# Performance work log

Hardware: AMD Instinct MI355X
Metric: run time of the kernel (lower is better)

The kernel has to match this reference:

```python
import jax, jax.numpy as jnp
import numpy as np

N_HEADS = 16


def _apply_rope(x, cos, sin):
    # x: (B, T, H, hd); cos/sin: (max_len, hd//2)
    B, T, H, hd = x.shape
    c = cos[:T][None, :, None, :]  # (1, T, 1, hd//2)
    s = sin[:T][None, :, None, :]
    x1 = x[..., 0::2]
    x2 = x[..., 1::2]
    y1 = x1 * c - x2 * s
    y2 = x1 * s + x2 * c
    return jnp.stack((y1, y2), axis=-1).reshape(B, T, H, hd)


def _precompute_rope(head_dim, max_len):
    theta = 10000.0
    inv = 1.0 / theta ** (np.arange(0, head_dim, 2, dtype=np.float32) / head_dim)
    t = np.arange(max_len, dtype=np.float32)
    freqs = np.outer(t, inv)
    return jnp.asarray(np.cos(freqs)), jnp.asarray(np.sin(freqs))


def setup_inputs() -> dict:
    key = jax.random.key(0)
    k1, k2, k3 = jax.random.split(key, 3)
    B, T, C = 4, 2048, 2048
    hd = C // N_HEADS
    x = jax.random.normal(k1, (B, T, C), dtype=jnp.float32)
    w_attn = jax.random.normal(k2, (C, 3 * C), dtype=jnp.float32) * (C ** -0.5)
    w_proj = jax.random.normal(k3, (C, C), dtype=jnp.float32) * (C ** -0.5)
    rope_cos, rope_sin = _precompute_rope(hd, T)
    return {"x": x, "w_attn": w_attn, "w_proj": w_proj,
            "rope_cos": rope_cos, "rope_sin": rope_sin}


def reference(x, w_attn, w_proj, rope_cos, rope_sin):
    B, T, C = x.shape
    H = N_HEADS
    hd = C // H
    qkv = x @ w_attn  # (B, T, 3C)
    q, k, v = jnp.split(qkv, 3, axis=2)
    q = q.reshape(B, T, H, hd)
    k = k.reshape(B, T, H, hd)
    v = v.reshape(B, T, H, hd)
    q = _apply_rope(q, rope_cos, rope_sin)
    k = _apply_rope(k, rope_cos, rope_sin)
    scale = 1.0 / jnp.sqrt(jnp.asarray(hd, dtype=x.dtype))
    scores = jnp.einsum('bqhd,bkhd->bhqk', q, k) * scale  # (B, H, T, T)
    causal = jnp.tril(jnp.ones((T, T), dtype=bool))
    scores = jnp.where(causal[None, None], scores, jnp.finfo(scores.dtype).min)
    attn = jax.nn.softmax(scores, axis=-1)
    y = jnp.einsum('bhqk,bkhd->bqhd', attn, v).reshape(B, T, C)
    return y @ w_proj
```

## Files before the change

### kernel.cpp

```cpp
#include <hip/hip_runtime.h>
#include <cstdint>
#include <cstddef>

#define DEVI __device__ __forceinline__

typedef __attribute__((ext_vector_type(8))) short bf16x8;
typedef __attribute__((ext_vector_type(4))) float f32x4;

DEVI unsigned short f2bf(float f) {
  unsigned int u = __float_as_uint(f);
  u += 0x7fffu + ((u >> 16) & 1u);
  return (unsigned short)(u >> 16);
}
DEVI float bf2f(unsigned int us) { return __uint_as_float(us << 16); }

DEVI void gld_lds16(const void* g, void* l) {
  __builtin_amdgcn_global_load_lds(
      (const __attribute__((address_space(1))) void*)g,
      (__attribute__((address_space(3))) void*)l, 16, 0, 0);
}

__global__ __launch_bounds__(256) void k_conv(const float* __restrict__ in,
                                              short* __restrict__ out, int n4) {
  int i = blockIdx.x * 256 + threadIdx.x;
  if (i >= n4) return;
  float4 v = reinterpret_cast<const float4*>(in)[i];
  uint2 o;
  o.x = (unsigned)f2bf(v.x) | ((unsigned)f2bf(v.y) << 16);
  o.y = (unsigned)f2bf(v.z) | ((unsigned)f2bf(v.w) << 16);
  reinterpret_cast<uint2*>(out)[i] = o;
}

__global__ __launch_bounds__(256) void k_transpose(const float* __restrict__ in,
                                                   short* __restrict__ out,
                                                   int R, int Cc) {
  __shared__ short tile[64][66];
  int tcols = Cc >> 6;
  int tb = blockIdx.x % tcols;
  int rb = blockIdx.x / tcols;
  int tid = threadIdx.x;
#pragma unroll
  for (int rep = 0; rep < 16; ++rep) {
    int idx = rep * 256 + tid;
    int r = idx >> 6, c = idx & 63;
    tile[r][c] = (short)f2bf(in[(size_t)(rb * 64 + r) * Cc + tb * 64 + c]);
  }
  __syncthreads();
#pragma unroll
  for (int rep = 0; rep < 16; ++rep) {
    int idx = rep * 256 + tid;
    int r = idx >> 6, c = idx & 63;
    out[(size_t)(tb * 64 + r) * R + rb * 64 + c] = tile[c][r];
  }
}

template <typename OutT>
__global__ __launch_bounds__(512, 2) void k_gemm8(const short* __restrict__ A,
                                                  const short* __restrict__ BT,
                                                  OutT* __restrict__ C,
                                                  int M, int N, int K) {
  __shared__ short sA[4][8192];
  __shared__ short sB[4][8192];
  const int tid = threadIdx.x;
  const int wv = tid >> 6, lane = tid & 63;
  const int l16 = lane & 15, lhi = lane >> 4;
  const int wr = wv >> 2, wc = wv & 3;
  const int bm = blockIdx.x * 256, bn = blockIdx.y * 256;
  const int srow0 = wv * 16 + (lane >> 2);
  const int sgs = lane & 3;
  const int NT = K >> 5;

  auto stageA = [&](int kt, int b) {
#pragma unroll
    for (int j = 0; j < 2; ++j) {
      int row = j * 128 + srow0;
      int g = sgs ^ ((row >> 1) & 3);
      gld_lds16(A + (size_t)(bm + row) * K + kt + g * 8,
                &sA[b][j * 4096 + wv * 512]);
    }
  };
  auto stageB = [&](int kt, int b) {
#pragma unroll
    for (int j = 0; j < 2; ++j) {
      int row = j * 128 + srow0;
      int g = sgs ^ ((row >> 1) & 3);
      gld_lds16(BT + (size_t)(bn + row) * K + kt + g * 8,
                &sB[b][j * 4096 + wv * 512]);
    }
  };

  f32x4 acc[8][4] = {};
  bf16x8 aP[8], bP[4], aQ[8], bQ[4];

#define FRAG_READ(DA, DB, BUF)                                                 \
  {                                                                            \
    const short* bufA_ = sA[(BUF)];                                            \
    const short* bufB_ = sB[(BUF)];                                            \
    _Pragma("unroll") for (int n = 0; n < 4; ++n) {                            \
      int row = wc * 64 + n * 16 + l16;                                        \
      DB[n] = *(const bf16x8*)&bufB_[row * 32 + ((lhi ^ ((row >> 1) & 3)) << 3)]; \
    }                                                                          \
    _Pragma("unroll") for (int m = 0; m < 8; ++m) {                            \
      int row = wr * 128 + m * 16 + l16;                                       \
      DA[m] = *(const bf16x8*)&bufA_[row * 32 + ((lhi ^ ((row >> 1) & 3)) << 3)]; \
    }                                                                          \
  }

#define TILE_BODY(T, CA, CB, NA, NB)                                           \
  {                                                                            \
    const int t_ = (T);                                                        \
    if (t_ + 1 < NT) FRAG_READ(NA, NB, (t_ + 1) & 3);                          \
    if (t_ + 3 < NT) {                                                         \
      stageA((t_ + 3) * 32, (t_ + 3) & 3);                                     \
      stageB((t_ + 3) * 32, (t_ + 3) & 3);                                     \
    }                                                                          \
    __builtin_amdgcn_sched_barrier(0);                                         \
    if (t_ + 3 < NT) {                                                         \
      asm volatile("s_waitcnt vmcnt(4)" ::: "memory");                         \
    } else {                                                                   \
      asm volatile("s_waitcnt vmcnt(0)" ::: "memory");                         \
    }                                                                          \
    __builtin_amdgcn_sched_barrier(0);                                         \
    __builtin_amdgcn_s_setprio(1);                                             \
    _Pragma("unroll") for (int m = 0; m < 8; ++m)                              \
        _Pragma("unroll") for (int n = 0; n < 4; ++n)                          \
            acc[m][n] = __builtin_amdgcn_mfma_f32_16x16x32_bf16(               \
                CA[m], CB[n], acc[m][n], 0, 0, 0);                             \
    __builtin_amdgcn_s_setprio(0);                                             \
    __builtin_amdgcn_sched_barrier(0);                                         \
    __builtin_amdgcn_s_barrier();                                              \
    __builtin_amdgcn_sched_barrier(0);                                         \
  }

  stageA(0, 0); stageB(0, 0);
  stageA(32, 1); stageB(32, 1);
  stageA(64, 2); stageB(64, 2);
  asm volatile("s_waitcnt vmcnt(8)" ::: "memory");
  __builtin_amdgcn_s_barrier();
  FRAG_READ(aP, bP, 0);
  asm volatile("s_waitcnt vmcnt(4)" ::: "memory");
  __builtin_amdgcn_s_barrier();
  __builtin_amdgcn_sched_barrier(0);

  for (int t = 0; t < NT; t += 2) {
    TILE_BODY(t, aP, bP, aQ, bQ);
    TILE_BODY(t + 1, aQ, bQ, aP, bP);
  }
#undef FRAG_READ
#undef TILE_BODY

#pragma unroll
  for (int m = 0; m < 8; ++m) {
#pragma unroll
    for (int n = 0; n < 4; ++n) {
      int col = bn + wc * 64 + n * 16 + l16;
#pragma unroll
      for (int r = 0; r < 4; ++r) {
        int row = bm + wr * 128 + m * 16 + lhi * 4 + r;
        if constexpr (sizeof(OutT) == 2)
          C[(size_t)row * N + col] = (OutT)f2bf(acc[m][n][r]);
        else
          C[(size_t)row * N + col] = acc[m][n][r];
      }
    }
  }
}

__global__ __launch_bounds__(256) void k_rope(const short* __restrict__ qkv,
                                              const float* __restrict__ cosb,
                                              const float* __restrict__ sinb,
                                              short* __restrict__ Qr,
                                              short* __restrict__ Kr) {
  const float kC = 0.08838834764831845f * 1.44269504088896340f;
  int gid = blockIdx.x * 4 + (threadIdx.x >> 6);
  int lane = threadIdx.x & 63;
  int h = gid & 15;
  int bt = gid >> 4;
  int t = bt & 2047;
  int b = bt >> 11;
  float c = cosb[t * 64 + lane];
  float s = sinb[t * 64 + lane];
  size_t qidx = (size_t)bt * 6144 + h * 128 + 2 * lane;
  size_t oidx = ((size_t)(b * 16 + h) * 2048 + t) * 128 + 2 * lane;
  unsigned int qp = *reinterpret_cast<const unsigned int*>(qkv + qidx);
  {
    float x1 = bf2f(qp & 0xffffu), x2 = bf2f(qp >> 16);
    unsigned int o = (unsigned)f2bf((x1 * c - x2 * s) * kC) |
                     ((unsigned)f2bf((x1 * s + x2 * c) * kC) << 16);
    *reinterpret_cast<unsigned int*>(Qr + oidx) = o;
  }
  unsigned int kp = *reinterpret_cast<const unsigned int*>(qkv + qidx + 2048);
  {
    float x1 = bf2f(kp & 0xffffu), x2 = bf2f(kp >> 16);
    unsigned int o = (unsigned)f2bf(x1 * c - x2 * s) |
                     ((unsigned)f2bf(x1 * s + x2 * c) << 16);
    *reinterpret_cast<unsigned int*>(Kr + oidx) = o;
  }
}

__global__ __launch_bounds__(256) void k_vtrans(const short* __restrict__ qkv,
                                                short* __restrict__ VT) {
  __shared__ short tile[64][66];
  int bh = blockIdx.x;
  int t0 = blockIdx.y * 64;
  int d0 = blockIdx.z * 64;
  int b = bh >> 4, h = bh & 15;
  int tid = threadIdx.x;
#pragma unroll
  for (int rep = 0; rep < 16; ++rep) {
    int idx = rep * 256 + tid;
    int r = idx >> 6, c = idx & 63;
    tile[r][c] = qkv[(size_t)(b * 2048 + t0 + r) * 6144 + 4096 + h * 128 + d0 + c];
  }
  __syncthreads();
#pragma unroll
  for (int rep = 0; rep < 16; ++rep) {
    int idx = rep * 256 + tid;
    int r = idx >> 6, c = idx & 63;
    VT[(size_t)(bh * 128 + d0 + r) * 2048 + t0 + c] = tile[c][r];
  }
}

__global__ __launch_bounds__(256) void k_attn(const short* __restrict__ Qr,
                                              const short* __restrict__ Kr,
                                              const short* __restrict__ VT,
                                              short* __restrict__ Y) {
  __shared__ short sK[2][64 * 128];
  __shared__ short sVT[2][128 * 64];
  __shared__ short sP[4][16 * 64];
  const int tid = threadIdx.x, wv = tid >> 6, lane = tid & 63;
  const int l8r = lane >> 3, l8c = lane & 7, l16 = lane & 15, lhi = lane >> 4;
  const int bid = blockIdx.x;
  const int pair = bid & 15, bh = bid >> 4;
  const size_t base = (size_t)bh * 2048 * 128;
  const int b = bh >> 4, h = bh & 15;

  const short ob = (short)0x3F80;
  const bf16x8 ones = {ob, ob, ob, ob, ob, ob, ob, ob};

  auto stage = [&](int kv0, int buf) {
#pragma unroll
    for (int rr = 0; rr < 4; ++rr) {
      int ch = rr * 4 + wv;
      {
        int row = ch * 4 + lhi;
        int wch = l16 ^ (row & 7);
        gld_lds16(Kr + base + (size_t)(kv0 + row) * 128 + wch * 8,
                  &sK[buf][ch * 512]);
      }
      {
        int drow = ch * 8 + l8r;
        int wch = l8c ^ (drow & 7);
        gld_lds16(VT + base + (size_t)drow * 2048 + kv0 + wch * 8,
                  &sVT[buf][ch * 512]);
      }
    }
  };

  for (int half = 0; half < 2; ++half) {
    const int qt = half ? 31 - pair : pair;
    const int q0 = qt * 64;
    const int nt = qt + 1;

    bf16x8 qf[4];
    const int qrow = q0 + wv * 16 + l16;
#pragma unroll
    for (int ks = 0; ks < 4; ++ks)
      qf[ks] = *reinterpret_cast<const bf16x8*>(Qr + base + (size_t)qrow * 128 +
                                                ks * 32 + lhi * 8);

    f32x4 acc_o[8] = {};
    f32x4 acc_l = {};
    float m_run[4];
#pragma unroll
    for (int r = 0; r < 4; ++r) m_run[r] = -1e30f;

    stage(0, 0);
    __syncthreads();

    for (int it = 0; it < nt; ++it) {
      const int cur = it & 1;
      if (it + 1 < nt) stage((it + 1) * 64, cur ^ 1);

      f32x4 sacc[4] = {};
#pragma unroll
      for (int cf = 0; cf < 4; ++cf) {
        int krow = cf * 16 + l16;
#pragma unroll
        for (int ks = 0; ks < 4; ++ks) {
          int e = krow * 128 + ks * 32 + lhi * 8;
          bf16x8 kf = *reinterpret_cast<const bf16x8*>(
              &sK[cur][e ^ ((krow & 7) << 3)]);
          sacc[cf] = __builtin_amdgcn_mfma_f32_16x16x32_bf16(qf[ks], kf,
                                                             sacc[cf], 0, 0, 0);
        }
      }

      if (it == nt - 1) {
#pragma unroll
        for (int cf = 0; cf < 4; ++cf) {
          int col = cf * 16 + l16;
#pragma unroll
          for (int r = 0; r < 4; ++r)
            if (col > wv * 16 + lhi * 4 + r) sacc[cf][r] = -3e38f;
        }
      }

      bool exceed = false;
#pragma unroll
      for (int cf = 0; cf < 4; ++cf)
#pragma unroll
        for (int r = 0; r < 4; ++r)
          exceed |= (sacc[cf][r] > m_run[r] + 8.f);

      if (__any(exceed)) {
        float resc[4];
#pragma unroll
        for (int r = 0; r < 4; ++r) {
          float mx = fmaxf(fmaxf(sacc[0][r], sacc[1][r]),
                           fmaxf(sacc[2][r], sacc[3][r]));
          mx = fmaxf(mx, __shfl_xor(mx, 1));
          mx = fmaxf(mx, __shfl_xor(mx, 2));
          mx = fmaxf(mx, __shfl_xor(mx, 4));
          mx = fmaxf(mx, __shfl_xor(mx, 8));
          float mnew = fmaxf(m_run[r], mx);
          resc[r] = exp2f(m_run[r] - mnew);
          m_run[r] = mnew;
        }
#pragma unroll
        for (int df = 0; df < 8; ++df)
#pragma unroll
          for (int r = 0; r < 4; ++r) acc_o[df][r] *= resc[r];
#pragma unroll
        for (int r = 0; r < 4; ++r) acc_l[r] *= resc[r];
      }

#pragma unroll
      for (int cf = 0; cf < 4; ++cf)
#pragma unroll
        for (int r = 0; r < 4; ++r) {
          float p = exp2f(sacc[cf][r] - m_run[r]);
          int prow = lhi * 4 + r;
          int e = prow * 64 + cf * 16 + l16;
          sP[wv][e ^ ((prow & 7) << 3)] = (short)f2bf(p);
        }

#pragma unroll
      for (int kk = 0; kk < 2; ++kk) {
        int e = l16 * 64 + kk * 32 + lhi * 8;
        bf16x8 pa = *reinterpret_cast<const bf16x8*>(
            &sP[wv][e ^ ((l16 & 7) << 3)]);
        acc_l = __builtin_amdgcn_mfma_f32_16x16x32_bf16(pa, ones, acc_l, 0, 0, 0);
#pragma unroll
        for (int df = 0; df < 8; ++df) {
          int vrow = df * 16 + l16;
          int ev = vrow * 64 + kk * 32 + lhi * 8;
          bf16x8 vb = *reinterpret_cast<const bf16x8*>(
              &sVT[cur][ev ^ ((vrow & 7) << 3)]);
          acc_o[df] = __builtin_amdgcn_mfma_f32_16x16x32_bf16(pa, vb,
                                                              acc_o[df], 0, 0, 0);
        }
      }
      __syncthreads();
    }

    float inv[4];
#pragma unroll
    for (int r = 0; r < 4; ++r) inv[r] = 1.f / acc_l[r];
#pragma unroll
    for (int df = 0; df < 8; ++df) {
      int col = h * 128 + df * 16 + l16;
#pragma unroll
      for (int r = 0; r < 4; ++r) {
        int row = q0 + wv * 16 + lhi * 4 + r;
        Y[((size_t)b * 2048 + row) * 2048 + col] =
            (short)f2bf(acc_o[df][r] * inv[r]);
      }
    }
  }
}

extern "C" void kernel_launch(void* const* d_in, const int* in_sizes, int n_in,
                              void* d_out, int out_size, void* d_ws, size_t ws_size,
                              hipStream_t stream) {
  const float* x        = (const float*)d_in[0];
  const float* w_attn   = (const float*)d_in[1];
  const float* w_proj   = (const float*)d_in[2];
  const float* rope_cos = (const float*)d_in[3];
  const float* rope_sin = (const float*)d_in[4];

  char* ws = (char*)d_ws;
  short* xbf    = (short*)(ws);
  short* wattnT = (short*)(ws + 33554432ull);
  short* wprojT = (short*)(ws + 58720256ull);
  short* qkv    = (short*)(ws + 67108864ull);
  short* Y      = qkv;
  short* Qr     = (short*)(ws + 167772160ull);
  short* Kr     = (short*)(ws + 201326592ull);
  short* VT     = (short*)(ws + 234881024ull);

  k_conv<<<16384, 256, 0, stream>>>(x, xbf, 4194304);
  k_transpose<<<3072, 256, 0, stream>>>(w_attn, wattnT, 2048, 6144);
  k_transpose<<<1024, 256, 0, stream>>>(w_proj, wprojT, 2048, 2048);
  k_gemm8<short><<<dim3(32, 24), 512, 0, stream>>>(xbf, wattnT, qkv,
                                                   8192, 6144, 2048);
  k_rope<<<32768, 256, 0, stream>>>(qkv, rope_cos, rope_sin, Qr, Kr);
  k_vtrans<<<dim3(64, 32, 2), 256, 0, stream>>>(qkv, VT);
  k_attn<<<1024, 256, 0, stream>>>(Qr, Kr, VT, Y);
  k_gemm8<float><<<dim3(32, 8), 512, 0, stream>>>(Y, wprojT, (float*)d_out,
                                                  8192, 2048, 2048);
}
```

Measured before the change: 496.0 us.

## Double query tile per attention block so each wave handles 32 query rows

```diff
diff --git a/kernel.cpp b/kernel.cpp
--- a/kernel.cpp
+++ b/kernel.cpp
@@ -227,11 +227,11 @@
                                               short* __restrict__ Y) {
   __shared__ short sK[2][64 * 128];
   __shared__ short sVT[2][128 * 64];
-  __shared__ short sP[4][16 * 64];
+  __shared__ short sP[4][32 * 64];
   const int tid = threadIdx.x, wv = tid >> 6, lane = tid & 63;
   const int l8r = lane >> 3, l8c = lane & 7, l16 = lane & 15, lhi = lane >> 4;
   const int bid = blockIdx.x;
-  const int pair = bid & 15, bh = bid >> 4;
+  const int pair = bid & 7, bh = bid >> 3;
   const size_t base = (size_t)bh * 2048 * 128;
   const int b = bh >> 4, h = bh & 15;
 
@@ -258,22 +258,27 @@
   };
 
   for (int half = 0; half < 2; ++half) {
-    const int qt = half ? 31 - pair : pair;
-    const int q0 = qt * 64;
-    const int nt = qt + 1;
-
-    bf16x8 qf[4];
-    const int qrow = q0 + wv * 16 + l16;
-#pragma unroll
-    for (int ks = 0; ks < 4; ++ks)
-      qf[ks] = *reinterpret_cast<const bf16x8*>(Qr + base + (size_t)qrow * 128 +
-                                                ks * 32 + lhi * 8);
-
-    f32x4 acc_o[8] = {};
-    f32x4 acc_l = {};
-    float m_run[4];
-#pragma unroll
-    for (int r = 0; r < 4; ++r) m_run[r] = -1e30f;
+    const int qt = half ? 15 - pair : pair;
+    const int q0 = qt * 128;
+    const int nt = 2 * qt + 2;
+
+    bf16x8 qf[2][4];
+#pragma unroll
+    for (int v = 0; v < 2; ++v) {
+      const int qrow = q0 + wv * 32 + v * 16 + l16;
+#pragma unroll
+      for (int ks = 0; ks < 4; ++ks)
+        qf[v][ks] = *reinterpret_cast<const bf16x8*>(
+            Qr + base + (size_t)qrow * 128 + ks * 32 + lhi * 8);
+    }
+
+    f32x4 acc_o[2][8] = {};
+    f32x4 acc_l[2] = {};
+    float m_run[2][4];
+#pragma unroll
+    for (int v = 0; v < 2; ++v)
+#pragma unroll
+      for (int r = 0; r < 4; ++r) m_run[v][r] = -1e30f;
 
     stage(0, 0);
     __syncthreads();
@@ -282,7 +287,7 @@
       const int cur = it & 1;
       if (it + 1 < nt) stage((it + 1) * 64, cur ^ 1);
 
-      f32x4 sacc[4] = {};
+      f32x4 sacc[2][4] = {};
 #pragma unroll
       for (int cf = 0; cf < 4; ++cf) {
         int krow = cf * 16 + l16;
@@ -291,90 +296,113 @@
           int e = krow * 128 + ks * 32 + lhi * 8;
           bf16x8 kf = *reinterpret_cast<const bf16x8*>(
               &sK[cur][e ^ ((krow & 7) << 3)]);
-          sacc[cf] = __builtin_amdgcn_mfma_f32_16x16x32_bf16(qf[ks], kf,
-                                                             sacc[cf], 0, 0, 0);
+          sacc[0][cf] = __builtin_amdgcn_mfma_f32_16x16x32_bf16(qf[0][ks], kf,
+                                                                sacc[0][cf], 0, 0, 0);
+          sacc[1][cf] = __builtin_amdgcn_mfma_f32_16x16x32_bf16(qf[1][ks], kf,
+                                                                sacc[1][cf], 0, 0, 0);
         }
       }
 
-      if (it == nt - 1) {
-#pragma unroll
-        for (int cf = 0; cf < 4; ++cf) {
-          int col = cf * 16 + l16;
+      if (it >= nt - 2) {
+        const int rel = it * 64 - q0;
+#pragma unroll
+        for (int v = 0; v < 2; ++v)
+#pragma unroll
+          for (int cf = 0; cf < 4; ++cf) {
+            int col = rel + cf * 16 + l16;
+#pragma unroll
+            for (int r = 0; r < 4; ++r)
+              if (col > wv * 32 + v * 16 + lhi * 4 + r) sacc[v][cf][r] = -3e38f;
+          }
+      }
+
+      bool exceed = false;
+#pragma unroll
+      for (int v = 0; v < 2; ++v)
+#pragma unroll
+        for (int cf = 0; cf < 4; ++cf)
 #pragma unroll
           for (int r = 0; r < 4; ++r)
-            if (col > wv * 16 + lhi * 4 + r) sacc[cf][r] = -3e38f;
+            exceed |= (sacc[v][cf][r] > m_run[v][r] + 8.f);
+
+      if (__any(exceed)) {
+#pragma unroll
+        for (int v = 0; v < 2; ++v) {
+          float resc[4];
+#pragma unroll
+          for (int r = 0; r < 4; ++r) {
+            float mx = fmaxf(fmaxf(sacc[v][0][r], sacc[v][1][r]),
+                             fmaxf(sacc[v][2][r], sacc[v][3][r]));
+            mx = fmaxf(mx, __shfl_xor(mx, 1));
+            mx = fmaxf(mx, __shfl_xor(mx, 2));
+            mx = fmaxf(mx, __shfl_xor(mx, 4));
+            mx = fmaxf(mx, __shfl_xor(mx, 8));
+            float mnew = fmaxf(m_run[v][r], mx);
+            resc[r] = exp2f(m_run[v][r] - mnew);
+            m_run[v][r] = mnew;
+          }
+#pragma unroll
+          for (int df = 0; df < 8; ++df)
+#pragma unroll
+            for (int r = 0; r < 4; ++r) acc_o[v][df][r] *= resc[r];
+#pragma unroll
+          for (int r = 0; r < 4; ++r) acc_l[v][r] *= resc[r];
         }
       }
 
-      bool exceed = false;
-#pragma unroll
-      for (int cf = 0; cf < 4; ++cf)
-#pragma unroll
-        for (int r = 0; r < 4; ++r)
-          exceed |= (sacc[cf][r] > m_run[r] + 8.f);
-
-      if (__any(exceed)) {
-        float resc[4];
-#pragma unroll
-        for (int r = 0; r < 4; ++r) {
-          float mx = fmaxf(fmaxf(sacc[0][r], sacc[1][r]),
-                           fmaxf(sacc[2][r], sacc[3][r]));
-          mx = fmaxf(mx, __shfl_xor(mx, 1));
-          mx = fmaxf(mx, __shfl_xor(mx, 2));
-          mx = fmaxf(mx, __shfl_xor(mx, 4));
-          mx = fmaxf(mx, __shfl_xor(mx, 8));
-          float mnew = fmaxf(m_run[r], mx);
-          resc[r] = exp2f(m_run[r] - mnew);
-          m_run[r] = mnew;
+#pragma unroll
+      for (int v = 0; v < 2; ++v)
+#pragma unroll
+        for (int cf = 0; cf < 4; ++cf)
+#pragma unroll
+          for (int r = 0; r < 4; ++r) {
+            float p = exp2f(sacc[v][cf][r] - m_run[v][r]);
+            int prow = v * 16 + lhi * 4 + r;
+            int e = prow * 64 + cf * 16 + l16;
+            sP[wv][e ^ ((prow & 7) << 3)] = (short)f2bf(p);
+          }
+
+#pragma unroll
+      for (int kk = 0; kk < 2; ++kk) {
+        bf16x8 pa[2];
+#pragma unroll
+        for (int v = 0; v < 2; ++v) {
+          int prow = v * 16 + l16;
+          int e = prow * 64 + kk * 32 + lhi * 8;
+          pa[v] = *reinterpret_cast<const bf16x8*>(
+              &sP[wv][e ^ ((prow & 7) << 3)]);
+          acc_l[v] = __builtin_amdgcn_mfma_f32_16x16x32_bf16(pa[v], ones,
+                                                             acc_l[v], 0, 0, 0);
         }
-#pragma unroll
-        for (int df = 0; df < 8; ++df)
-#pragma unroll
-          for (int r = 0; r < 4; ++r) acc_o[df][r] *= resc[r];
-#pragma unroll
-        for (int r = 0; r < 4; ++r) acc_l[r] *= resc[r];
-      }
-
-#pragma unroll
-      for (int cf = 0; cf < 4; ++cf)
-#pragma unroll
-        for (int r = 0; r < 4; ++r) {
-          float p = exp2f(sacc[cf][r] - m_run[r]);
-          int prow = lhi * 4 + r;
-          int e = prow * 64 + cf * 16 + l16;
-          sP[wv][e ^ ((prow & 7) << 3)] = (short)f2bf(p);
-        }
-
-#pragma unroll
-      for (int kk = 0; kk < 2; ++kk) {
-        int e = l16 * 64 + kk * 32 + lhi * 8;
-        bf16x8 pa = *reinterpret_cast<const bf16x8*>(
-            &sP[wv][e ^ ((l16 & 7) << 3)]);
-        acc_l = __builtin_amdgcn_mfma_f32_16x16x32_bf16(pa, ones, acc_l, 0, 0, 0);
 #pragma unroll
         for (int df = 0; df < 8; ++df) {
           int vrow = df * 16 + l16;
           int ev = vrow * 64 + kk * 32 + lhi * 8;
           bf16x8 vb = *reinterpret_cast<const bf16x8*>(
               &sVT[cur][ev ^ ((vrow & 7) << 3)]);
-          acc_o[df] = __builtin_amdgcn_mfma_f32_16x16x32_bf16(pa, vb,
-                                                              acc_o[df], 0, 0, 0);
+          acc_o[0][df] = __builtin_amdgcn_mfma_f32_16x16x32_bf16(pa[0], vb,
+                                                                 acc_o[0][df], 0, 0, 0);
+          acc_o[1][df] = __builtin_amdgcn_mfma_f32_16x16x32_bf16(pa[1], vb,
+                                                                 acc_o[1][df], 0, 0, 0);
         }
       }
       __syncthreads();
     }
 
-    float inv[4];
-#pragma unroll
-    for (int r = 0; r < 4; ++r) inv[r] = 1.f / acc_l[r];
-#pragma unroll
-    for (int df = 0; df < 8; ++df) {
-      int col = h * 128 + df * 16 + l16;
-#pragma unroll
-      for (int r = 0; r < 4; ++r) {
-        int row = q0 + wv * 16 + lhi * 4 + r;
-        Y[((size_t)b * 2048 + row) * 2048 + col] =
-            (short)f2bf(acc_o[df][r] * inv[r]);
+#pragma unroll
+    for (int v = 0; v < 2; ++v) {
+      float inv[4];
+#pragma unroll
+      for (int r = 0; r < 4; ++r) inv[r] = 1.f / acc_l[v][r];
+#pragma unroll
+      for (int df = 0; df < 8; ++df) {
+        int col = h * 128 + df * 16 + l16;
+#pragma unroll
+        for (int r = 0; r < 4; ++r) {
+          int row = q0 + wv * 32 + v * 16 + lhi * 4 + r;
+          Y[((size_t)b * 2048 + row) * 2048 + col] =
+              (short)f2bf(acc_o[v][df][r] * inv[r]);
+        }
       }
     }
   }
@@ -406,7 +434,7 @@
                                                    8192, 6144, 2048);
   k_rope<<<32768, 256, 0, stream>>>(qkv, rope_cos, rope_sin, Qr, Kr);
   k_vtrans<<<dim3(64, 32, 2), 256, 0, stream>>>(qkv, VT);
-  k_attn<<<1024, 256, 0, stream>>>(Qr, Kr, VT, Y);
+  k_attn<<<512, 256, 0, stream>>>(Qr, Kr, VT, Y);
   k_gemm8<float><<<dim3(32, 8), 512, 0, stream>>>(Y, wprojT, (float*)d_out,
                                                   8192, 2048, 2048);
 }
```

After: 521.7 us. 5.2% more time.

## Fuse RoPE and V transpose into the QKV GEMM epilogue

Applied to the files above, without the earlier changes.

```diff
diff --git a/kernel.cpp b/kernel.cpp
--- a/kernel.cpp
+++ b/kernel.cpp
@@ -54,11 +54,16 @@
   }
 }
 
-template <typename OutT>
+template <int MODE, typename OutT>
 __global__ __launch_bounds__(512, 2) void k_gemm8(const short* __restrict__ A,
                                                   const short* __restrict__ BT,
                                                   OutT* __restrict__ C,
-                                                  int M, int N, int K) {
+                                                  int M, int N, int K,
+                                                  const float* __restrict__ cosb,
+                                                  const float* __restrict__ sinb,
+                                                  short* __restrict__ Qr,
+                                                  short* __restrict__ Kr,
+                                                  short* __restrict__ VT) {
   __shared__ short sA[4][8192];
   __shared__ short sB[4][8192];
   const int tid = threadIdx.x;
@@ -149,75 +154,64 @@
 #undef FRAG_READ
 #undef TILE_BODY
 
-#pragma unroll
-  for (int m = 0; m < 8; ++m) {
-#pragma unroll
-    for (int n = 0; n < 4; ++n) {
-      int col = bn + wc * 64 + n * 16 + l16;
-#pragma unroll
-      for (int r = 0; r < 4; ++r) {
-        int row = bm + wr * 128 + m * 16 + lhi * 4 + r;
-        if constexpr (sizeof(OutT) == 2)
-          C[(size_t)row * N + col] = (OutT)f2bf(acc[m][n][r]);
-        else
+  if constexpr (MODE == 1) {
+#pragma unroll
+    for (int m = 0; m < 8; ++m) {
+#pragma unroll
+      for (int n = 0; n < 4; ++n) {
+        int col = bn + wc * 64 + n * 16 + l16;
+#pragma unroll
+        for (int r = 0; r < 4; ++r) {
+          int row = bm + wr * 128 + m * 16 + lhi * 4 + r;
           C[(size_t)row * N + col] = acc[m][n][r];
-      }
-    }
-  }
-}
-
-__global__ __launch_bounds__(256) void k_rope(const short* __restrict__ qkv,
-                                              const float* __restrict__ cosb,
-                                              const float* __restrict__ sinb,
-                                              short* __restrict__ Qr,
-                                              short* __restrict__ Kr) {
-  const float kC = 0.08838834764831845f * 1.44269504088896340f;
-  int gid = blockIdx.x * 4 + (threadIdx.x >> 6);
-  int lane = threadIdx.x & 63;
-  int h = gid & 15;
-  int bt = gid >> 4;
-  int t = bt & 2047;
-  int b = bt >> 11;
-  float c = cosb[t * 64 + lane];
-  float s = sinb[t * 64 + lane];
-  size_t qidx = (size_t)bt * 6144 + h * 128 + 2 * lane;
-  size_t oidx = ((size_t)(b * 16 + h) * 2048 + t) * 128 + 2 * lane;
-  unsigned int qp = *reinterpret_cast<const unsigned int*>(qkv + qidx);
-  {
-    float x1 = bf2f(qp & 0xffffu), x2 = bf2f(qp >> 16);
-    unsigned int o = (unsigned)f2bf((x1 * c - x2 * s) * kC) |
-                     ((unsigned)f2bf((x1 * s + x2 * c) * kC) << 16);
-    *reinterpret_cast<unsigned int*>(Qr + oidx) = o;
-  }
-  unsigned int kp = *reinterpret_cast<const unsigned int*>(qkv + qidx + 2048);
-  {
-    float x1 = bf2f(kp & 0xffffu), x2 = bf2f(kp >> 16);
-    unsigned int o = (unsigned)f2bf(x1 * c - x2 * s) |
-                     ((unsigned)f2bf(x1 * s + x2 * c) << 16);
-    *reinterpret_cast<unsigned int*>(Kr + oidx) = o;
-  }
-}
-
-__global__ __launch_bounds__(256) void k_vtrans(const short* __restrict__ qkv,
-                                                short* __restrict__ VT) {
-  __shared__ short tile[64][66];
-  int bh = blockIdx.x;
-  int t0 = blockIdx.y * 64;
-  int d0 = blockIdx.z * 64;
-  int b = bh >> 4, h = bh & 15;
-  int tid = threadIdx.x;
-#pragma unroll
-  for (int rep = 0; rep < 16; ++rep) {
-    int idx = rep * 256 + tid;
-    int r = idx >> 6, c = idx & 63;
-    tile[r][c] = qkv[(size_t)(b * 2048 + t0 + r) * 6144 + 4096 + h * 128 + d0 + c];
-  }
-  __syncthreads();
-#pragma unroll
-  for (int rep = 0; rep < 16; ++rep) {
-    int idx = rep * 256 + tid;
-    int r = idx >> 6, c = idx & 63;
-    VT[(size_t)(bh * 128 + d0 + r) * 2048 + t0 + c] = tile[c][r];
+        }
+      }
+    }
+  } else {
+    const int part = bn >> 11;
+    const float kC = 0.08838834764831845f * 1.44269504088896340f;
+    if (part < 2) {
+      const float qs = (part == 0) ? kC : 1.0f;
+      short* dst = (part == 0) ? Qr : Kr;
+#pragma unroll
+      for (int m = 0; m < 8; ++m) {
+#pragma unroll
+        for (int n = 0; n < 4; ++n) {
+          int colm = (bn & 2047) + wc * 64 + n * 16 + l16;
+          int h = colm >> 7, d = colm & 127;
+          int p = d >> 1;
+          bool ev = (d & 1) == 0;
+#pragma unroll
+          for (int r = 0; r < 4; ++r) {
+            int row = bm + wr * 128 + m * 16 + lhi * 4 + r;
+            int b = row >> 11, t = row & 2047;
+            float c = cosb[t * 64 + p];
+            float s = sinb[t * 64 + p];
+            float x = acc[m][n][r];
+            float xp = __shfl_xor(x, 1);
+            float y = ev ? (x * c - xp * s) : (xp * s + x * c);
+            dst[((size_t)(b * 16 + h) * 2048 + t) * 128 + d] =
+                (short)f2bf(y * qs);
+          }
+        }
+      }
+    } else {
+#pragma unroll
+      for (int m = 0; m < 8; ++m) {
+#pragma unroll
+        for (int n = 0; n < 4; ++n) {
+          int colm = (bn & 2047) + wc * 64 + n * 16 + l16;
+          int h = colm >> 7, d = colm & 127;
+#pragma unroll
+          for (int r = 0; r < 4; ++r) {
+            int row = bm + wr * 128 + m * 16 + lhi * 4 + r;
+            int b = row >> 11, t = row & 2047;
+            VT[((size_t)(b * 16 + h) * 128 + d) * 2048 + t] =
+                (short)f2bf(acc[m][n][r]);
+          }
+        }
+      }
+    }
   }
 }
 
@@ -393,8 +387,7 @@
   short* xbf    = (short*)(ws);
   short* wattnT = (short*)(ws + 33554432ull);
   short* wprojT = (short*)(ws + 58720256ull);
-  short* qkv    = (short*)(ws + 67108864ull);
-  short* Y      = qkv;
+  short* Y      = (short*)(ws + 67108864ull);
   short* Qr     = (short*)(ws + 167772160ull);
   short* Kr     = (short*)(ws + 201326592ull);
   short* VT     = (short*)(ws + 234881024ull);
@@ -402,11 +395,11 @@
   k_conv<<<16384, 256, 0, stream>>>(x, xbf, 4194304);
   k_transpose<<<3072, 256, 0, stream>>>(w_attn, wattnT, 2048, 6144);
   k_transpose<<<1024, 256, 0, stream>>>(w_proj, wprojT, 2048, 2048);
-  k_gemm8<short><<<dim3(32, 24), 512, 0, stream>>>(xbf, wattnT, qkv,
-                                                   8192, 6144, 2048);
-  k_rope<<<32768, 256, 0, stream>>>(qkv, rope_cos, rope_sin, Qr, Kr);
-  k_vtrans<<<dim3(64, 32, 2), 256, 0, stream>>>(qkv, VT);
+  k_gemm8<2, short><<<dim3(32, 24), 512, 0, stream>>>(
+      xbf, wattnT, (short*)nullptr, 8192, 6144, 2048,
+      rope_cos, rope_sin, Qr, Kr, VT);
   k_attn<<<1024, 256, 0, stream>>>(Qr, Kr, VT, Y);
-  k_gemm8<float><<<dim3(32, 8), 512, 0, stream>>>(Y, wprojT, (float*)d_out,
-                                                  8192, 2048, 2048);
-}
+  k_gemm8<1, float><<<dim3(32, 8), 512, 0, stream>>>(
+      Y, wprojT, (float*)d_out, 8192, 2048, 2048,
+      nullptr, nullptr, nullptr, nullptr, nullptr);
+}
```

Measured after the change: 473.1 us. -4.6%, faster.
